# Performance work log

Hardware: AMD Instinct MI355X
Metric: run time of the kernel (lower is better)

## Reference

```python
import jax, jax.numpy as jnp
import numpy as np

B, S, IB, H = 256, 64, 32, 4
PB = 6                      # ceil(log2(max_seq_len=64)) position bits (BINARY mode)
SIM_IN = 2 * IB + 2 * PB    # similarity RAM input bits = 76
SIM_BITS = 12               # min(SIM_IN, 12) address bits per similarity neuron
VAL_IN = IB + PB            # value RAM input bits = 38
VAL_BITS = 10               # min(VAL_IN, 10)
OUT_IN = H * IB             # output RAM input bits = 128
OUT_BITS = 12               # min(OUT_IN, 12)


def _bin_enc(pos, nbits):
    # [S] -> [S, nbits] MSB-first binary position encoding
    shifts = jnp.arange(nbits - 1, -1, -1)
    return ((pos[:, None] >> shifts[None, :]) & 1).astype(jnp.int32)


def setup_inputs() -> dict:
    key = jax.random.key(0)
    ks = jax.random.split(key, 8)
    tokens = jax.random.randint(ks[0], (B, S, IB), 0, 2, dtype=jnp.int32)
    sim_conn = jax.random.randint(ks[1], (H, SIM_BITS), 0, SIM_IN, dtype=jnp.int32)
    sim_mem = jax.random.bernoulli(ks[2], 0.5, (H, 2 ** SIM_BITS)).astype(jnp.float32)
    val_conn = jax.random.randint(ks[3], (H, IB, VAL_BITS), 0, VAL_IN, dtype=jnp.int32)
    val_mem = jax.random.bernoulli(ks[4], 0.5, (H, IB, 2 ** VAL_BITS)).astype(jnp.float32)
    agg_mem = jax.random.bernoulli(ks[5], 0.5, (H, IB, S + 1)).astype(jnp.float32)
    out_conn = jax.random.randint(ks[6], (IB, OUT_BITS), 0, OUT_IN, dtype=jnp.int32)
    out_mem = jax.random.bernoulli(ks[7], 0.5, (IB, 2 ** OUT_BITS)).astype(jnp.float32)
    return dict(tokens=tokens, sim_conn=sim_conn, sim_mem=sim_mem, val_conn=val_conn,
                val_mem=val_mem, agg_mem=agg_mem, out_conn=out_conn, out_mem=out_mem)


def reference(tokens, sim_conn, sim_mem, val_conn, val_mem, agg_mem, out_conn, out_mem):
    pos = jnp.arange(S)
    pb = _bin_enc(pos, PB)                                        # [S, PB]
    # ---- similarity heads: binary (hard) attention pattern ----------------
    qb = jnp.broadcast_to(tokens[:, :, None, :], (B, S, S, IB))
    kb = jnp.broadcast_to(tokens[:, None, :, :], (B, S, S, IB))
    qp = jnp.broadcast_to(pb[None, :, None, :], (B, S, S, PB))
    kp = jnp.broadcast_to(pb[None, None, :, :], (B, S, S, PB))
    pair = jnp.concatenate([qb, kb, qp, kp], axis=-1)             # [B,S,S,SIM_IN]
    sim_bits = pair[..., sim_conn]                                # [B,S,S,H,SIM_BITS]
    w_sim = (2 ** jnp.arange(SIM_BITS - 1, -1, -1)).astype(jnp.int32)
    sim_addr = (sim_bits * w_sim).sum(-1)                         # [B,S,S,H]
    attend = sim_mem[jnp.arange(H)[None, None, None, :], sim_addr]  # {0,1}
    causal = (pos[:, None] >= pos[None, :]).astype(attend.dtype)    # attend only j <= i
    attention = attend * causal[None, :, :, None]                 # [B,S,S,H]
    # ---- value heads: RAM projection of (token bits, key position bits) ---
    val_in = jnp.concatenate([tokens, jnp.broadcast_to(pb[None], (B, S, PB))], axis=-1)
    val_bits = val_in[..., val_conn]                              # [B,S,H,IB,VAL_BITS]
    w_val = (2 ** jnp.arange(VAL_BITS - 1, -1, -1)).astype(jnp.int32)
    val_addr = (val_bits * w_val).sum(-1)                         # [B,S,H,IB]
    proj = val_mem[jnp.arange(H)[None, None, :, None],
                   jnp.arange(IB)[None, None, None, :], val_addr]  # [B,S,H,IB]
    # ---- learned aggregation: order-invariant per-bit vote counts -> RAM --
    counts = jnp.einsum('bijh,bjhn->bihn', attention, proj)       # [B,S,H,IB]
    n_att = attention.sum(2)                                      # [B,S,H]
    cnt_idx = jnp.clip(jnp.round(counts), 0, S).astype(jnp.int32)
    agg = agg_mem[jnp.arange(H)[None, None, :, None],
                  jnp.arange(IB)[None, None, None, :], cnt_idx]   # [B,S,H,IB]
    agg = jnp.where(n_att[..., None] > 0.5, agg, 0.0)             # nothing attended -> zeros
    # ---- output RAM layer over concatenated head outputs ------------------
    combined = agg.reshape(B, S, H * IB)                          # [B,S,OUT_IN]
    out_bits = combined[..., out_conn]                            # [B,S,IB,OUT_BITS]
    w_out = (2.0 ** jnp.arange(OUT_BITS - 1, -1, -1)).astype(combined.dtype)
    out_addr = jnp.clip(jnp.round((out_bits * w_out).sum(-1)), 0, 2 ** OUT_BITS - 1).astype(jnp.int32)
    return out_mem[jnp.arange(IB)[None, None, :], out_addr]       # [B,S,IB]
```

## Files before the change

### kernel.cpp

```cpp
#include <hip/hip_runtime.h>
#include <stdint.h>

constexpr int NB = 256;
constexpr int NS = 64;
constexpr int NIB = 32;
constexpr int NH = 4;
constexpr int SIMB = 12;
constexpr int VALB = 10;
constexpr int OUTB = 12;

__global__ __launch_bounds__(1024) void ram_direct(
    const int* __restrict__ tokens,
    const int* __restrict__ sim_conn,
    const float* __restrict__ sim_mem,
    const int* __restrict__ val_conn,
    const float* __restrict__ val_mem,
    const float* __restrict__ agg_mem,
    const int* __restrict__ out_conn,
    const float* __restrict__ out_mem,
    float* __restrict__ out)
{
    const int b = blockIdx.x;
    const int tid = threadIdx.x, lane = tid & 63, wave = tid >> 6;

    __shared__ uint32_t s_tok[NS];
    __shared__ int      s_sconn[NH * SIMB];
    __shared__ int      s_vconn[NH * NIB * VALB];
    __shared__ int      s_oconn[NIB * OUTB];
    __shared__ uint32_t s_ip[NS][NH];
    __shared__ uint32_t s_jp[NS][NH];
    __shared__ uint64_t s_att[NS][NH];
    __shared__ uint64_t s_proj[NH][NIB];
    __shared__ uint32_t s_comb[NS][NH];

    {
        const int base = b * (NS * NIB);
#pragma unroll
        for (int r = 0; r < 2; ++r) {
            const int e = r * 1024 + tid;
            uint64_t m = __ballot(tokens[base + e] & 1);
            if (lane == 0) {
                int w = e >> 5;
                s_tok[w]     = (uint32_t)m;
                s_tok[w + 1] = (uint32_t)(m >> 32);
            }
        }
    }
    if (tid < NH * SIMB) s_sconn[tid] = sim_conn[tid];
    for (int i = tid; i < NH * NIB * VALB; i += 1024) s_vconn[i] = val_conn[i];
    if (tid >= 640) s_oconn[tid - 640] = out_conn[tid - 640];
    __syncthreads();

    const uint32_t tkj = s_tok[lane];
    const uint32_t rev6 = __brev((uint32_t)lane) >> 26;
    const uint64_t V = (uint64_t)tkj | ((uint64_t)rev6 << 32);

    if (tid < 256) {
        const int s = tid >> 2, h = tid & 3;
        const uint32_t tk = s_tok[s];
        uint32_t ip = 0, jp = 0;
#pragma unroll
        for (int t = 0; t < SIMB; ++t) {
            int c = s_sconn[h * SIMB + t];
            uint32_t w = 1u << (SIMB - 1 - t);
            if (c < 32)      ip += ((tk >> c) & 1u) * w;
            else if (c < 64) jp += ((tk >> (c - 32)) & 1u) * w;
            else if (c < 70) ip += (((uint32_t)s >> (69 - c)) & 1u) * w;
            else             jp += (((uint32_t)s >> (75 - c)) & 1u) * w;
        }
        s_ip[s][h] = ip;
        s_jp[s][h] = jp;
    }

    for (int r = 0; r < 8; ++r) {
        const int hn = wave * 8 + r;
        const int* conn = s_vconn + hn * VALB;
        uint32_t addr = 0;
#pragma unroll
        for (int t = 0; t < VALB; ++t)
            addr += (uint32_t)((V >> conn[t]) & 1ull) << (VALB - 1 - t);
        uint64_t m = __ballot(val_mem[hn * 1024 + addr] > 0.5f);
        if (lane == 0) s_proj[hn >> 5][hn & 31] = m;
    }
    __syncthreads();

    for (int r = 0; r < 16; ++r) {
        const int idx = wave * 16 + r;
        const int i = idx >> 2, h = idx & 3;
        uint32_t addr = s_ip[i][h] + s_jp[lane][h];
        uint64_t m = __ballot(sim_mem[h * 4096 + addr] > 0.5f);
        if (lane == 0) s_att[i][h] = m & (~0ull >> (63 - i));
    }
    __syncthreads();

    {
        const int i = tid >> 4, h = (tid >> 2) & 3, q = tid & 3;
        const uint64_t am = s_att[i][h];
        uint32_t word = 0;
#pragma unroll
        for (int nn = 0; nn < 8; ++nn) {
            const int n = q * 8 + nn;
            int cnt = __popcll(am & s_proj[h][n]);
            uint32_t bit = (agg_mem[(h * NIB + n) * (NS + 1) + cnt] > 0.5f) ? 1u : 0u;
            word |= bit << n;
        }
        word = (am != 0ull) ? word : 0u;
        word |= __shfl_xor(word, 1);
        word |= __shfl_xor(word, 2);
        if (q == 0) s_comb[i][h] = word;
    }
    __syncthreads();

    {
        const int n = tid & 31;
        const int ii = tid >> 5;
        int conn[OUTB];
#pragma unroll
        for (int t = 0; t < OUTB; ++t) conn[t] = s_oconn[n * OUTB + t];
        const float* om = out_mem + n * 4096;
#pragma unroll
        for (int k = 0; k < 2; ++k) {
            const int i = ii + k * 32;
            uint64_t lo = (uint64_t)s_comb[i][0] | ((uint64_t)s_comb[i][1] << 32);
            uint64_t hi = (uint64_t)s_comb[i][2] | ((uint64_t)s_comb[i][3] << 32);
            uint32_t addr = 0;
#pragma unroll
            for (int t = 0; t < OUTB; ++t) {
                int c = conn[t];
                uint64_t w = (c < 64) ? lo : hi;
                addr += (uint32_t)((w >> (c & 63)) & 1ull) << (OUTB - 1 - t);
            }
            out[(b * NS + i) * NIB + n] = om[addr];
        }
    }
}

extern "C" void kernel_launch(void* const* d_in, const int* in_sizes, int n_in,
                              void* d_out, int out_size, void* d_ws, size_t ws_size,
                              hipStream_t stream) {
    const int*   tokens   = (const int*)d_in[0];
    const int*   sim_conn = (const int*)d_in[1];
    const float* sim_mem  = (const float*)d_in[2];
    const int*   val_conn = (const int*)d_in[3];
    const float* val_mem  = (const float*)d_in[4];
    const float* agg_mem  = (const float*)d_in[5];
    const int*   out_conn = (const int*)d_in[6];
    const float* out_mem  = (const float*)d_in[7];
    float* out = (float*)d_out;
    (void)d_ws; (void)ws_size; (void)in_sizes; (void)n_in; (void)out_size;

    ram_direct<<<NB, 1024, 0, stream>>>(tokens, sim_conn, sim_mem, val_conn,
                                        val_mem, agg_mem, out_conn, out_mem, out);
}
```

Measured before the change: 19.36 us.

## Compute similarity partial addresses in registers and exchange via wave shuffles

Drops the shared-memory staging of the connection tables and of the per-position similarity partial addresses. Each lane now computes the query/key partial addresses for its own position in registers, and the query part for a row is fetched with a wave shuffle. This removes one block barrier and the shared-memory round trips. In exchange every thread reads the connection arrays straight from global memory (uniform, cached loads) and does redundant address computation for all four heads.

```diff
diff --git a/kernel.cpp b/kernel.cpp
--- a/kernel.cpp
+++ b/kernel.cpp
@@ -9,7 +9,7 @@
 constexpr int VALB = 10;
 constexpr int OUTB = 12;
 
-__global__ __launch_bounds__(1024) void ram_direct(
+__global__ __launch_bounds__(1024) void ram_v2(
     const int* __restrict__ tokens,
     const int* __restrict__ sim_conn,
     const float* __restrict__ sim_mem,
@@ -24,11 +24,6 @@
     const int tid = threadIdx.x, lane = tid & 63, wave = tid >> 6;
 
     __shared__ uint32_t s_tok[NS];
-    __shared__ int      s_sconn[NH * SIMB];
-    __shared__ int      s_vconn[NH * NIB * VALB];
-    __shared__ int      s_oconn[NIB * OUTB];
-    __shared__ uint32_t s_ip[NS][NH];
-    __shared__ uint32_t s_jp[NS][NH];
     __shared__ uint64_t s_att[NS][NH];
     __shared__ uint64_t s_proj[NH][NIB];
     __shared__ uint32_t s_comb[NS][NH];
@@ -46,35 +41,33 @@
             }
         }
     }
-    if (tid < NH * SIMB) s_sconn[tid] = sim_conn[tid];
-    for (int i = tid; i < NH * NIB * VALB; i += 1024) s_vconn[i] = val_conn[i];
-    if (tid >= 640) s_oconn[tid - 640] = out_conn[tid - 640];
     __syncthreads();
 
     const uint32_t tkj = s_tok[lane];
     const uint32_t rev6 = __brev((uint32_t)lane) >> 26;
     const uint64_t V = (uint64_t)tkj | ((uint64_t)rev6 << 32);
 
-    if (tid < 256) {
-        const int s = tid >> 2, h = tid & 3;
-        const uint32_t tk = s_tok[s];
+    uint32_t ipl[NH], jpl[NH];
+#pragma unroll
+    for (int h = 0; h < NH; ++h) {
         uint32_t ip = 0, jp = 0;
 #pragma unroll
         for (int t = 0; t < SIMB; ++t) {
-            int c = s_sconn[h * SIMB + t];
+            int c = sim_conn[h * SIMB + t];
             uint32_t w = 1u << (SIMB - 1 - t);
-            if (c < 32)      ip += ((tk >> c) & 1u) * w;
-            else if (c < 64) jp += ((tk >> (c - 32)) & 1u) * w;
-            else if (c < 70) ip += (((uint32_t)s >> (69 - c)) & 1u) * w;
-            else             jp += (((uint32_t)s >> (75 - c)) & 1u) * w;
+            if (c < 32)      ip += ((tkj >> c) & 1u) * w;
+            else if (c < 64) jp += ((tkj >> (c - 32)) & 1u) * w;
+            else if (c < 70) ip += (((uint32_t)lane >> (69 - c)) & 1u) * w;
+            else             jp += (((uint32_t)lane >> (75 - c)) & 1u) * w;
         }
-        s_ip[s][h] = ip;
-        s_jp[s][h] = jp;
+        ipl[h] = ip;
+        jpl[h] = jp;
     }
 
+#pragma unroll
     for (int r = 0; r < 8; ++r) {
         const int hn = wave * 8 + r;
-        const int* conn = s_vconn + hn * VALB;
+        const int* conn = val_conn + hn * VALB;
         uint32_t addr = 0;
 #pragma unroll
         for (int t = 0; t < VALB; ++t)
@@ -82,12 +75,13 @@
         uint64_t m = __ballot(val_mem[hn * 1024 + addr] > 0.5f);
         if (lane == 0) s_proj[hn >> 5][hn & 31] = m;
     }
-    __syncthreads();
 
+#pragma unroll
     for (int r = 0; r < 16; ++r) {
-        const int idx = wave * 16 + r;
-        const int i = idx >> 2, h = idx & 3;
-        uint32_t addr = s_ip[i][h] + s_jp[lane][h];
+        const int h = r & 3;
+        const int i = wave * 4 + (r >> 2);
+        uint32_t ipv = (uint32_t)__shfl((int)ipl[h], i);
+        uint32_t addr = ipv + jpl[h];
         uint64_t m = __ballot(sim_mem[h * 4096 + addr] > 0.5f);
         if (lane == 0) s_att[i][h] = m & (~0ull >> (63 - i));
     }
@@ -116,7 +110,7 @@
         const int ii = tid >> 5;
         int conn[OUTB];
 #pragma unroll
-        for (int t = 0; t < OUTB; ++t) conn[t] = s_oconn[n * OUTB + t];
+        for (int t = 0; t < OUTB; ++t) conn[t] = out_conn[n * OUTB + t];
         const float* om = out_mem + n * 4096;
 #pragma unroll
         for (int k = 0; k < 2; ++k) {
@@ -149,6 +143,6 @@
     float* out = (float*)d_out;
     (void)d_ws; (void)ws_size; (void)in_sizes; (void)n_in; (void)out_size;
 
-    ram_direct<<<NB, 1024, 0, stream>>>(tokens, sim_conn, sim_mem, val_conn,
-                                        val_mem, agg_mem, out_conn, out_mem, out);
+    ram_v2<<<NB, 1024, 0, stream>>>(tokens, sim_conn, sim_mem, val_conn,
+                                    val_mem, agg_mem, out_conn, out_mem, out);
 }
```

Measured after the change: 23.35 us. +20.6%, slower.
